# Performance work log

Hardware: AMD Instinct MI355X
Metric: run time of the kernel (lower is better)

Reference implementation:

```python
import jax, jax.numpy as jnp
import numpy as np

N_HEADS = 32
N_KV = 8
N_REP = N_HEADS // N_KV  # 4
HD = 128
ROPE_THETA = 500000.0


def _rope_tables(seq_len, hd, theta):
    inv = 1.0 / (theta ** (np.arange(0, hd, 2, dtype=np.float32) / hd))  # [hd/2]
    t = np.arange(seq_len, dtype=np.float32)
    ang = np.outer(t, inv)  # [T, hd/2]
    return jnp.asarray(np.cos(ang)), jnp.asarray(np.sin(ang))


def setup_inputs() -> dict:
    key = jax.random.key(0)
    ks = jax.random.split(key, 8)
    B, T, D = 2, 2048, 4096
    s = 0.02
    x = jax.random.normal(ks[0], (B, T, D), jnp.float32)
    wq = jax.random.normal(ks[1], (D, D), jnp.float32) * s
    wk = jax.random.normal(ks[2], (N_KV * HD, D), jnp.float32) * s
    wv = jax.random.normal(ks[3], (N_KV * HD, D), jnp.float32) * s
    wo = jax.random.normal(ks[4], (D, D), jnp.float32) * s
    cache_k = jnp.zeros((B, T, N_KV, HD), jnp.float32)
    cache_v = jnp.zeros((B, T, N_KV, HD), jnp.float32)
    cos, sin = _rope_tables(T, HD, ROPE_THETA)
    mask = jnp.zeros((1,), jnp.float32)  # accepted by forward but never applied
    return {"x": x, "wq": wq, "wk": wk, "wv": wv, "wo": wo,
            "cache_k": cache_k, "cache_v": cache_v,
            "cos": cos, "sin": sin, "mask": mask, "start_pos": 0}


def _apply_rope(t, cos, sin):
    # t: [B, T, H, HD]; pairs (t0,t1) along last dim act as complex numbers
    tr = t.reshape(*t.shape[:-1], HD // 2, 2)
    re, im = tr[..., 0], tr[..., 1]
    c = cos[None, :, None, :]  # [1,T,1,HD/2]
    s = sin[None, :, None, :]
    out = jnp.stack([re * c - im * s, re * s + im * c], axis=-1)
    return out.reshape(t.shape)


def reference(x, wq, wk, wv, wo, cache_k, cache_v, cos, sin, mask, start_pos):
    B, T, D = x.shape
    q = (x @ wq.T).reshape(B, T, N_HEADS, HD)
    k = (x @ wk.T).reshape(B, T, N_KV, HD)
    v = (x @ wv.T).reshape(B, T, N_KV, HD)

    q = _apply_rope(q, cos, sin)
    k = _apply_rope(k, cos, sin)

    # KV-cache write (start_pos is a python int)
    cache_k = cache_k.at[:, start_pos:start_pos + T].set(k)
    cache_v = cache_v.at[:, start_pos:start_pos + T].set(v)
    keys = cache_k[:, :start_pos + T]   # [B,S,Kv,HD]
    vals = cache_v[:, :start_pos + T]

    # GQA attention without materializing repeat_kv: q head h uses kv head h // N_REP
    q5 = q.reshape(B, T, N_KV, N_REP, HD)
    scale = 1.0 / jnp.sqrt(jnp.float32(HD))
    scores = jnp.einsum('btkrd,bskd->bkrts', q5, keys) * scale  # [B,Kv,Rep,T,S]
    # NOTE: source forward never adds `mask` to scores; faithfully omitted.
    probs = jax.nn.softmax(scores, axis=-1)
    ctx = jnp.einsum('bkrts,bskd->btkrd', probs, vals)  # [B,T,Kv,Rep,HD]
    cat = ctx.reshape(B, T, N_HEADS * HD)
    return cat @ wo.T
```

## Files before the change

kernel.cpp:

```cpp
#include <hip/hip_runtime.h>
#include <hip/hip_bf16.h>
#include <stdint.h>


typedef short bf16x8 __attribute__((ext_vector_type(8)));
typedef float f32x4  __attribute__((ext_vector_type(4)));

#define GLB_AS(p) ((__attribute__((address_space(1))) void*)(p))
#define LDS_AS(p) ((__attribute__((address_space(3))) void*)(p))

__device__ __forceinline__ float bf2f(ushort u) {
    union { unsigned int i; float f; } v; v.i = ((unsigned int)u) << 16; return v.f;
}
__device__ __forceinline__ ushort f2bf(float f) {
    union { float f; unsigned int i; } v; v.f = f;
    unsigned int r = v.i + 0x7FFFu + ((v.i >> 16) & 1u);
    return (ushort)(r >> 16);
}
__device__ __forceinline__ unsigned int pk_bf16(float a, float b) {
    return (unsigned int)f2bf(a) | ((unsigned int)f2bf(b) << 16);
}
__device__ __forceinline__ unsigned int cvtpk2(float lo, float hi) {
    unsigned int r;
    asm("v_cvt_pk_bf16_f32 %0, %1, %2" : "=v"(r) : "v"(lo), "v"(hi));
    return r;
}
__device__ __forceinline__ void store_c(ushort* p, float v) { *p = f2bf(v); }
__device__ __forceinline__ void store_c(float*  p, float v) { *p = v; }

__device__ __forceinline__ void barr() {
    asm volatile("" ::: "memory");
    __builtin_amdgcn_s_barrier();
    asm volatile("" ::: "memory");
}

__global__ __launch_bounds__(256) void cast_f2b(
    const float4* __restrict__ src, ushort4* __restrict__ dst, int n4)
{
    int i = blockIdx.x * 256 + threadIdx.x;
    if (i < n4) {
        float4 v = src[i];
        ushort4 o;
        o.x = f2bf(v.x); o.y = f2bf(v.y); o.z = f2bf(v.z); o.w = f2bf(v.w);
        dst[i] = o;
    }
}

enum { OFF_A0 = 0, OFF_A1 = 16384, OFF_B0 = 32768, OFF_B1 = 49152, BUFSZ = 65536 };

__device__ __forceinline__ void rdA(const char* half, bf16x8 (&a)[4][2],
                                    int wm, int quad, int l16) {
    const int cx = l16 & 7;
#pragma unroll
    for (int m2 = 0; m2 < 4; m2++)
#pragma unroll
        for (int ks = 0; ks < 2; ks++)
            a[m2][ks] = *(const bf16x8*)(half + (wm * 64 + m2 * 16 + l16) * 128
                                              + (((ks * 4 + quad) ^ cx) * 16));
}
__device__ __forceinline__ void rdB(const char* half, bf16x8 (&b)[2][2],
                                    int wn, int quad, int l16) {
    const int cx = l16 & 7;
#pragma unroll
    for (int n2 = 0; n2 < 2; n2++)
#pragma unroll
        for (int ks = 0; ks < 2; ks++)
            b[n2][ks] = *(const bf16x8*)(half + (wn * 32 + n2 * 16 + l16) * 128
                                              + (((ks * 4 + quad) ^ cx) * 16));
}
template <int MH, int NH>
__device__ __forceinline__ void mmq(f32x4 (&acc)[2][2][4][2],
                                    const bf16x8 (&a)[4][2], const bf16x8 (&b)[2][2]) {
    __builtin_amdgcn_s_setprio(1);
#pragma unroll
    for (int m2 = 0; m2 < 4; m2++)
#pragma unroll
        for (int n2 = 0; n2 < 2; n2++)
#pragma unroll
            for (int ks = 0; ks < 2; ks++)
                acc[MH][NH][m2][n2] = __builtin_amdgcn_mfma_f32_16x16x32_bf16(
                    a[m2][ks], b[n2][ks], acc[MH][NH][m2][n2], 0, 0, 0);
    __builtin_amdgcn_s_setprio(0);
}
__device__ __forceinline__ void stage_half(const char* src, char* dst, size_t kb) {
    __builtin_amdgcn_global_load_lds(GLB_AS(src),           LDS_AS(dst),        16, 0, 0);
    __builtin_amdgcn_global_load_lds(GLB_AS(src + 64 * kb), LDS_AS(dst + 8192), 16, 0, 0);
}

#define GATE8 asm volatile("s_waitcnt vmcnt(8)" ::: "memory")
#define GATE0 asm volatile("s_waitcnt vmcnt(0)" ::: "memory")
#define GATEN ((void)0)

#define DO_TILE(LBUF, KO, DO_STAGE, GATE)                                        \
    {                                                                            \
        const char* Lb = lds + (LBUF) * BUFSZ;                                   \
        char* Sb = ldsW + (LBUF) * BUFSZ;                                        \
                                                         \
        rdA(Lb + OFF_A0, a, wm, quad, l16);                                      \
        rdB(Lb + OFF_B0, b0, wn, quad, l16);                                     \
        barr();                                                                  \
        mmq<0, 0>(acc, a, b0);                                                   \
        barr();                                                                  \
                                       \
        rdB(Lb + OFF_B1, b1, wn, quad, l16);                                     \
        if (DO_STAGE) {                                                          \
            stage_half(aSrc + (KO), Sb + OFF_A0, kb);                            \
            stage_half(bSrc + (KO), Sb + OFF_B0, kb);                            \
        }                                                                        \
        barr();                                                                  \
        mmq<0, 1>(acc, a, b1);                                                   \
        barr();                                                                  \
                      \
        rdA(Lb + OFF_A1, a, wm, quad, l16);                                      \
        if (DO_STAGE) stage_half(bSrc + 128 * kb + (KO), Sb + OFF_B1, kb);       \
        barr();                                                                  \
        mmq<1, 1>(acc, a, b1);                                                   \
        barr();                                                                  \
                             \
        if (DO_STAGE) stage_half(aSrc + 128 * kb + (KO), Sb + OFF_A1, kb);       \
        barr();                                                                  \
        mmq<1, 0>(acc, a, b0);                                                   \
        GATE;                                                                    \
        barr();                                                                  \
    }

template <typename OT>
__global__ __launch_bounds__(512, 2) void gemm_nt256(
    const ushort* __restrict__ A, const ushort* __restrict__ B,
    OT* __restrict__ C, int N, int K)
{
    __shared__ __align__(16) char lds[131072];

    const int tid = threadIdx.x, lane = tid & 63, w = tid >> 6;
    const int wm = w >> 2, wn = w & 3;
    const int quad = lane >> 4, l16 = lane & 15;

    const int nwg = gridDim.x;
    const int swz = ((int)blockIdx.x & 7) * (nwg >> 3) + ((int)blockIdx.x >> 3);
    const int nx  = N >> 8;
    const int bm  = (swz / nx) * 256, bn = (swz % nx) * 256;

    const size_t kb = (size_t)K * 2;

    const int srow = tid >> 3;
    const int gch  = (tid & 7) ^ (srow & 7);
    const char* aSrc = (const char*)A + (size_t)(bm + srow) * kb + gch * 16;
    const char* bSrc = (const char*)B + (size_t)(bn + srow) * kb + gch * 16;
    char* ldsW = lds + w * 1024;

    f32x4 acc[2][2][4][2];
#pragma unroll
    for (int i = 0; i < 2; i++)
#pragma unroll
        for (int j = 0; j < 2; j++)
#pragma unroll
            for (int m2 = 0; m2 < 4; m2++)
#pragma unroll
                for (int n2 = 0; n2 < 2; n2++)
                    acc[i][j][m2][n2] = (f32x4){0.f, 0.f, 0.f, 0.f};

    bf16x8 a[4][2], b0[2][2], b1[2][2];

    stage_half(aSrc,                ldsW + OFF_A0, kb);
    stage_half(aSrc + 128 * kb,     ldsW + OFF_A1, kb);
    stage_half(bSrc,                ldsW + OFF_B0, kb);
    stage_half(bSrc + 128 * kb,     ldsW + OFF_B1, kb);
    stage_half(aSrc + 128,            ldsW + BUFSZ + OFF_A0, kb);
    stage_half(aSrc + 128 * kb + 128, ldsW + BUFSZ + OFF_A1, kb);
    stage_half(bSrc + 128,            ldsW + BUFSZ + OFF_B0, kb);
    stage_half(bSrc + 128 * kb + 128, ldsW + BUFSZ + OFF_B1, kb);
    GATE8;
    barr();

    int ko = 256;
    for (int it = 0; it < 31; ++it, ko += 256) {
        DO_TILE(0, ko,       true, GATE8);
        DO_TILE(1, ko + 128, true, GATE8);
    }
    DO_TILE(0, 0, false, GATE0);
    DO_TILE(1, 0, false, GATEN);

#pragma unroll
    for (int MH = 0; MH < 2; MH++)
#pragma unroll
        for (int NH = 0; NH < 2; NH++)
#pragma unroll
            for (int m2 = 0; m2 < 4; m2++)
#pragma unroll
                for (int n2 = 0; n2 < 2; n2++)
#pragma unroll
                    for (int r = 0; r < 4; r++) {
                        int row = bm + MH * 128 + wm * 64 + m2 * 16 + quad * 4 + r;
                        int col = bn + NH * 128 + wn * 32 + n2 * 16 + l16;
                        store_c(&C[(size_t)row * N + col], acc[MH][NH][m2][n2][r]);
                    }
}

__global__ __launch_bounds__(256) void rope_kernel(
    ushort* __restrict__ X, const float* __restrict__ cosv,
    const float* __restrict__ sinv, int ldx, int tprs, float scale)
{
    int gid = blockIdx.x * 256 + threadIdx.x;
    int m  = gid >> tprs;
    int pi = (gid & ((1 << tprs) - 1)) * 4;
    int t  = m & 2047;
    int i  = pi & 63;
    float4 c4 = *(const float4*)&cosv[t * 64 + i];
    float4 s4 = *(const float4*)&sinv[t * 64 + i];
    ushort* px = X + (size_t)m * ldx + pi * 2;
    uint4 d = *(const uint4*)px;
    unsigned int parts[4] = {d.x, d.y, d.z, d.w};
    float cc[4] = {c4.x, c4.y, c4.z, c4.w};
    float ss[4] = {s4.x, s4.y, s4.z, s4.w};
#pragma unroll
    for (int p = 0; p < 4; p++) {
        float re = bf2f((ushort)(parts[p] & 0xffffu));
        float im = bf2f((ushort)(parts[p] >> 16));
        float re2 = (re * cc[p] - im * ss[p]) * scale;
        float im2 = (re * ss[p] + im * cc[p]) * scale;
        parts[p] = pk_bf16(re2, im2);
    }
    *(uint4*)px = make_uint4(parts[0], parts[1], parts[2], parts[3]);
}

__global__ __launch_bounds__(256) void transpose_v(
    const ushort* __restrict__ KV, ushort* __restrict__ Vt)
{
    __shared__ ushort tile[32][33];
    int n0 = blockIdx.x * 32, m0 = blockIdx.y * 32;
    int tx = threadIdx.x & 31, ty = threadIdx.x >> 5;
#pragma unroll
    for (int r = ty; r < 32; r += 8)
        tile[r][tx] = KV[(size_t)(m0 + r) * 2048 + 1024 + n0 + tx];
    __syncthreads();
    int b  = m0 >> 11;
    int t0 = m0 & 2047;
#pragma unroll
    for (int r = ty; r < 32; r += 8)
        Vt[(size_t)b * 2097152 + (size_t)(n0 + r) * 2048 + t0 + tx] = tile[tx][r];
}

__global__ __launch_bounds__(512) void flash_attn(
    const ushort* __restrict__ Q, const ushort* __restrict__ KV,
    const ushort* __restrict__ Vt, ushort* __restrict__ ctx)
{
    __shared__ __align__(16) ushort lK[64 * 128];
    __shared__ __align__(16) ushort lV[128 * 64];
    __shared__ __align__(16) ushort lP[8 * 16 * 72];

    const int qt = blockIdx.x, h = blockIdx.y, b = blockIdx.z;
    const int kv = h >> 2;
    const int tid = threadIdx.x, lane = tid & 63, w = tid >> 6;
    const int quad = lane >> 4, l16 = lane & 15;

    const int q0 = qt * 128 + w * 16;
    const size_t qrow = (size_t)(b * 2048 + q0 + l16) * 4096 + h * 128;
    bf16x8 bQ[4];
#pragma unroll
    for (int ks = 0; ks < 4; ks++)
        bQ[ks] = *(const bf16x8*)&Q[qrow + ks * 32 + quad * 8];

    f32x4 o[8];
#pragma unroll
    for (int dc = 0; dc < 8; dc++) o[dc] = (f32x4){0.f, 0.f, 0.f, 0.f};
    float m = -1e30f, l = 0.f;

    const ushort* gK = KV + (size_t)(b * 2048) * 2048 + kv * 128;
    const ushort* gV = Vt + (size_t)(b * 8 + kv) * 2048 * 128;
    ushort* pw = &lP[w * 16 * 72];

    const int keyb = tid >> 4, dsub = tid & 15;
    const int db   = tid >> 3, ssub = tid & 7;
    const ushort* baseK = gK + (size_t)keyb * 2048 + (dsub ^ (keyb & 15)) * 8;
    const ushort* baseV = gV + (size_t)db * 2048 + (ssub ^ (db & 7)) * 8;
    char* ldsK = (char*)lK + (tid & 448) * 16;
    char* ldsV = (char*)lV + (tid & 448) * 16;

    for (int s0 = 0; s0 < 2048; s0 += 64) {
#pragma unroll
        for (int rep = 0; rep < 2; rep++) {
            __builtin_amdgcn_global_load_lds(
                GLB_AS(baseK + (size_t)(s0 + rep * 32) * 2048),
                LDS_AS(ldsK + rep * 8192), 16, 0, 0);
            __builtin_amdgcn_global_load_lds(
                GLB_AS(baseV + (size_t)rep * 131072 + s0),
                LDS_AS(ldsV + rep * 8192), 16, 0, 0);
        }
        __syncthreads();

        f32x4 scT[4];
#pragma unroll
        for (int g = 0; g < 4; g++) scT[g] = (f32x4){0.f, 0.f, 0.f, 0.f};
#pragma unroll
        for (int g = 0; g < 4; g++)
#pragma unroll
            for (int ks = 0; ks < 4; ks++) {
                bf16x8 aK = *(const bf16x8*)&lK[(g * 16 + l16) * 128 + ((ks * 4 + quad) ^ l16) * 8];
                scT[g] = __builtin_amdgcn_mfma_f32_16x16x32_bf16(aK, bQ[ks], scT[g], 0, 0, 0);
            }

        float tmax = scT[0][0];
#pragma unroll
        for (int g = 0; g < 4; g++)
#pragma unroll
            for (int r = 0; r < 4; r++) tmax = fmaxf(tmax, scT[g][r]);
        tmax = fmaxf(tmax, __shfl_xor(tmax, 16, 64));
        tmax = fmaxf(tmax, __shfl_xor(tmax, 32, 64));

        if (__any(tmax > m + 8.f)) {
            float mnew = fmaxf(m, tmax);
            float alpha = exp2f(m - mnew);
            m = mnew;
            l *= alpha;
#pragma unroll
            for (int dc = 0; dc < 8; dc++)
#pragma unroll
                for (int r = 0; r < 4; r++) o[dc][r] *= alpha;
        }

        float p[16];
        float ts = 0.f;
#pragma unroll
        for (int i = 0; i < 16; i++) {
            p[i] = exp2f(scT[i >> 2][i & 3] - m);
            ts += p[i];
        }
        ts += __shfl_xor(ts, 16, 64);
        ts += __shfl_xor(ts, 32, 64);
        l += ts;

#pragma unroll
        for (int g = 0; g < 4; g++) {
            uint2 pk;
            pk.x = cvtpk2(p[g * 4 + 0], p[g * 4 + 1]);
            pk.y = cvtpk2(p[g * 4 + 2], p[g * 4 + 3]);
            *(uint2*)&pw[l16 * 72 + g * 16 + quad * 4] = pk;
        }
        bf16x8 bP[2];
#pragma unroll
        for (int c = 0; c < 2; c++)
            bP[c] = *(const bf16x8*)&pw[l16 * 72 + c * 32 + quad * 8];

#pragma unroll
        for (int dc = 0; dc < 8; dc++)
#pragma unroll
            for (int c = 0; c < 2; c++) {
                bf16x8 aV = *(const bf16x8*)&lV[(dc * 16 + l16) * 64 + ((c * 4 + quad) ^ (l16 & 7)) * 8];
                o[dc] = __builtin_amdgcn_mfma_f32_16x16x32_bf16(aV, bP[c], o[dc], 0, 0, 0);
            }
        __syncthreads();
    }

    float inv = 1.0f / l;
#pragma unroll
    for (int dc = 0; dc < 8; dc++) {
        uint2 pk;
        pk.x = cvtpk2(o[dc][0] * inv, o[dc][1] * inv);
        pk.y = cvtpk2(o[dc][2] * inv, o[dc][3] * inv);
        *(uint2*)&ctx[qrow + dc * 16 + quad * 4] = pk;
    }
}

extern "C" void kernel_launch(void* const* d_in, const int* in_sizes, int n_in,
                              void* d_out, int out_size, void* d_ws, size_t ws_size,
                              hipStream_t stream)
{
    const float* x    = (const float*)d_in[0];
    const float* wq   = (const float*)d_in[1];
    const float* wk   = (const float*)d_in[2];
    const float* wv   = (const float*)d_in[3];
    const float* wo   = (const float*)d_in[4];
    const float* cosv = (const float*)d_in[7];
    const float* sinv = (const float*)d_in[8];
    float* out = (float*)d_out;

    ushort* Xb   = (ushort*)d_ws;
    ushort* ctx  = Xb;
    ushort* Wbig = Xb   + (size_t)16 * 1024 * 1024;
    ushort* Wsm  = Wbig + (size_t)16 * 1024 * 1024;
    ushort* Vt   = Wsm;
    ushort* Q    = Wsm  + (size_t)8  * 1024 * 1024;
    ushort* KV   = Q    + (size_t)16 * 1024 * 1024;

    dim3 blk(256);
    cast_f2b<<<16384, blk, 0, stream>>>((const float4*)x,  (ushort4*)Xb,   4194304);
    cast_f2b<<<16384, blk, 0, stream>>>((const float4*)wq, (ushort4*)Wbig, 4194304);
    cast_f2b<<<4096,  blk, 0, stream>>>((const float4*)wk, (ushort4*)Wsm,  1048576);
    cast_f2b<<<4096,  blk, 0, stream>>>((const float4*)wv, (ushort4*)(Wsm + (size_t)4194304), 1048576);

    gemm_nt256<<<dim3(256), dim3(512), 0, stream>>>(Xb, Wbig, Q,  4096, 4096);
    gemm_nt256<<<dim3(128), dim3(512), 0, stream>>>(Xb, Wsm,  KV, 2048, 4096);

    cast_f2b<<<16384, blk, 0, stream>>>((const float4*)wo, (ushort4*)Wbig, 4194304);

    rope_kernel<<<8192, blk, 0, stream>>>(Q,  cosv, sinv, 4096, 9,
                                          0.08838834764831845f * 1.4426950408889634f);
    rope_kernel<<<2048, blk, 0, stream>>>(KV, cosv, sinv, 2048, 7, 1.0f);
    transpose_v<<<dim3(32, 128), blk, 0, stream>>>(KV, Vt);

    flash_attn<<<dim3(16, 32, 2), dim3(512), 0, stream>>>(Q, KV, Vt, ctx);

    gemm_nt256<<<dim3(256), dim3(512), 0, stream>>>(ctx, Wbig, out, 4096, 4096);
}
```

Before: 771.8 us.

## Overlap next K/V tile loads with attention compute using split staging

Splits the K and V LDS staging into separate lambdas and prefetches the next K tile while the PV MFMAs run, then the next V tile once they finish, with explicit vmcnt waits and barriers. This aims to hide global-to-LDS load latency that was previously fully exposed at the start of each iteration. The row-max reduction is also rewritten as a tree to shorten the dependency chain. It adds barriers per iteration and relies on the existing barr() helper and on careful vmcnt accounting, so any ordering mistake could corrupt data.

```diff
diff --git a/kernel.cpp b/kernel.cpp
--- a/kernel.cpp
+++ b/kernel.cpp
@@ -276,17 +276,28 @@
     char* ldsK = (char*)lK + (tid & 448) * 16;
     char* ldsV = (char*)lV + (tid & 448) * 16;
 
-    for (int s0 = 0; s0 < 2048; s0 += 64) {
-#pragma unroll
-        for (int rep = 0; rep < 2; rep++) {
+    auto STAGE_K = [&](int s0) {
+#pragma unroll
+        for (int rep = 0; rep < 2; rep++)
             __builtin_amdgcn_global_load_lds(
                 GLB_AS(baseK + (size_t)(s0 + rep * 32) * 2048),
                 LDS_AS(ldsK + rep * 8192), 16, 0, 0);
+    };
+    auto STAGE_V = [&](int s0) {
+#pragma unroll
+        for (int rep = 0; rep < 2; rep++)
             __builtin_amdgcn_global_load_lds(
                 GLB_AS(baseV + (size_t)rep * 131072 + s0),
                 LDS_AS(ldsV + rep * 8192), 16, 0, 0);
-        }
-        __syncthreads();
+    };
+
+    STAGE_K(0);
+    STAGE_V(0);
+    asm volatile("s_waitcnt vmcnt(2)" ::: "memory");
+    barr();
+
+    for (int it = 0; it < 32; ++it) {
+        const int s0 = it * 64;
 
         f32x4 scT[4];
 #pragma unroll
@@ -299,11 +310,11 @@
                 scT[g] = __builtin_amdgcn_mfma_f32_16x16x32_bf16(aK, bQ[ks], scT[g], 0, 0, 0);
             }
 
-        float tmax = scT[0][0];
-#pragma unroll
-        for (int g = 0; g < 4; g++)
-#pragma unroll
-            for (int r = 0; r < 4; r++) tmax = fmaxf(tmax, scT[g][r]);
+        float m0a = fmaxf(fmaxf(scT[0][0], scT[0][1]), fmaxf(scT[0][2], scT[0][3]));
+        float m1a = fmaxf(fmaxf(scT[1][0], scT[1][1]), fmaxf(scT[1][2], scT[1][3]));
+        float m2a = fmaxf(fmaxf(scT[2][0], scT[2][1]), fmaxf(scT[2][2], scT[2][3]));
+        float m3a = fmaxf(fmaxf(scT[3][0], scT[3][1]), fmaxf(scT[3][2], scT[3][3]));
+        float tmax = fmaxf(fmaxf(m0a, m1a), fmaxf(m2a, m3a));
         tmax = fmaxf(tmax, __shfl_xor(tmax, 16, 64));
         tmax = fmaxf(tmax, __shfl_xor(tmax, 32, 64));
 
@@ -341,6 +352,10 @@
         for (int c = 0; c < 2; c++)
             bP[c] = *(const bf16x8*)&pw[l16 * 72 + c * 32 + quad * 8];
 
+        asm volatile("s_waitcnt vmcnt(0)" ::: "memory");
+        barr();
+        if (it < 31) STAGE_K(s0 + 64);
+
 #pragma unroll
         for (int dc = 0; dc < 8; dc++)
 #pragma unroll
@@ -348,7 +363,12 @@
                 bf16x8 aV = *(const bf16x8*)&lV[(dc * 16 + l16) * 64 + ((c * 4 + quad) ^ (l16 & 7)) * 8];
                 o[dc] = __builtin_amdgcn_mfma_f32_16x16x32_bf16(aV, bP[c], o[dc], 0, 0, 0);
             }
-        __syncthreads();
+        barr();
+        if (it < 31) {
+            STAGE_V(s0 + 64);
+            asm volatile("s_waitcnt vmcnt(2)" ::: "memory");
+        }
+        barr();
     }
 
     float inv = 1.0f / l;
```

Measured after the change: 774.6 us. No clear change (+0.4%).
